# Kernel tuning notes

Hardware: AMD Instinct MI355X
Metric: run time of the kernel (lower is better)

## Reference

```python
import jax, jax.numpy as jnp
import numpy as np

N = 100000   # nodes
E = 3200000  # edges (avg degree 32)
D = 128      # in_dim
RATIO = 0.5
K = int(RATIO * N)  # nodes kept by pooling


def setup_inputs() -> dict:
    key = jax.random.key(0)
    k1, k2, k3 = jax.random.split(key, 3)
    x = jax.random.normal(k1, (N, D), dtype=jnp.float32)
    edge_index = jax.random.randint(k2, (2, E), 0, N, dtype=jnp.int32)
    weight = jax.random.normal(k3, (D, D), dtype=jnp.float32) / np.sqrt(D)
    bias = jnp.zeros((D,), dtype=jnp.float32)
    return {"x": x, "edge_index": edge_index, "weight": weight, "bias": bias}


def gcn_conv(x, edge_index, weight, bias):
    # PyG GCNConv: out = D^{-1/2} (A + I) D^{-1/2} X W + b
    h = x @ weight  # [N, D]
    src, dst = edge_index[0], edge_index[1]
    deg = jax.ops.segment_sum(jnp.ones((E,), h.dtype), dst, num_segments=N) + 1.0  # self-loop
    dinv = jax.lax.rsqrt(deg)  # [N]
    norm = dinv[src] * dinv[dst]  # [E]
    msg = h[src] * norm[:, None]  # gather + scale
    agg = jax.ops.segment_sum(msg, dst, num_segments=N)  # scatter-add
    agg = agg + h * (dinv * dinv)[:, None]  # self-loop contribution
    return agg + bias


def reference(x, edge_index, weight, bias):
    h = gcn_conv(x, edge_index, weight, bias)  # [N, D] node scores/features
    score = jnp.sqrt(jnp.sum(h * h, axis=-1) + 1e-12)  # scalar score per node
    _, perm = jax.lax.top_k(score, K)  # top-k node selection
    x_out = h[perm] * jnp.tanh(score[perm])[:, None]  # gated gather of kept nodes
    # remap / filter edges to the induced subgraph (jit-safe: padded with mask)
    pos = jnp.full((N,), -1, dtype=jnp.int32).at[perm].set(jnp.arange(K, dtype=jnp.int32))
    new_src = pos[edge_index[0]]
    new_dst = pos[edge_index[1]]
    edge_mask = (new_src >= 0) & (new_dst >= 0)
    new_edge_index = jnp.where(edge_mask[None, :], jnp.stack([new_src, new_dst]), -1)
    return x_out, new_edge_index, edge_mask
```

## Files before the change

### kernel.cpp

```cpp
#include <hip/hip_runtime.h>
#include <hip/hip_fp16.h>
#include <stdint.h>

#define NN 100000
#define EE 3200000
#define DD 128
#define KK 50000
#define NB 32768
#define SBLK 128
#define BB 2048
#define NBK 391
#define TILE 8192
#define BMAX 12288
#define NBLK 391

using u16 = unsigned short;
using u32 = unsigned int;
using u64 = unsigned long long;

typedef _Float16 f16x8 __attribute__((ext_vector_type(8)));
typedef float f32x4 __attribute__((ext_vector_type(4)));

__device__ __forceinline__ float bq(float f) {
  u32 b = __float_as_uint(f);
  b += 0x7FFFu + ((b >> 16) & 1u);
  return __uint_as_float(b & 0xFFFF0000u);
}

__device__ __forceinline__ u32 packh2(float a, float b) {
  return (u32)__half_as_ushort(__float2half(a)) |
         ((u32)__half_as_ushort(__float2half(b)) << 16);
}

__global__ void k_init(u32* __restrict__ chist, u32* __restrict__ bcnt,
                       u64* __restrict__ meta, u32* __restrict__ mflag) {
  int i = blockIdx.x * 256 + threadIdx.x;
  for (int j = i; j < NB; j += 256 * 256) bcnt[j] = 0u;
  if (i < NBK) chist[i] = 0u;
  if (i == 0) { meta[0] = ~0ull; meta[1] = 0ull; *mflag = 0u; }
}

__global__ void k_chist(const int* __restrict__ ei, u32* __restrict__ chist) {
  __shared__ u32 cnt[NBK];
  int t = threadIdx.x;
  int e0 = blockIdx.x * TILE;
  int vcnt = EE - e0; if (vcnt > TILE) vcnt = TILE;
  for (int i = t; i < NBK; i += 256) cnt[i] = 0;
  __syncthreads();
  for (int i = t; i < vcnt; i += 256)
    atomicAdd(&cnt[(u32)ei[EE + e0 + i] >> 8], 1u);
  __syncthreads();
  for (int i = t; i < NBK; i += 256)
    if (cnt[i]) atomicAdd(&chist[i], cnt[i]);
}

__global__ void k_cscan(const u32* __restrict__ chist, u32* __restrict__ cbase,
                        u32* __restrict__ pbcur) {
  __shared__ u32 buf[2][512];
  int t = threadIdx.x;
  u32 v = (t < NBK) ? chist[t] : 0u;
  int a = 0; buf[0][t] = v; __syncthreads();
  for (int s = 1; s < 512; s <<= 1) {
    buf[1 - a][t] = buf[a][t] + ((t >= s) ? buf[a][t - s] : 0u);
    a = 1 - a; __syncthreads();
  }
  if (t < NBK) { u32 e = buf[a][t] - v; cbase[t] = e; pbcur[t] = e; }
}

__global__ void k_part1(const int* __restrict__ ei, u32* __restrict__ bcur,
                        u32* __restrict__ ebuf) {
  __shared__ u32 cnt[NBK];
  __shared__ u32 lpos[NBK];
  __shared__ u32 gbase[NBK];
  __shared__ u32 sbuf[TILE];
  __shared__ u16 sbid[TILE];
  int t = threadIdx.x;
  int e0 = blockIdx.x * TILE;
  int vcnt = EE - e0; if (vcnt > TILE) vcnt = TILE;
  for (int i = t; i < NBK; i += 256) cnt[i] = 0;
  __syncthreads();
  for (int i = t; i < vcnt; i += 256) {
    int d = ei[EE + e0 + i];
    atomicAdd(&cnt[d >> 8], 1u);
  }
  __syncthreads();
  if (t < 64) {
    u32 carry = 0;
    for (int c = 0; c < 7; ++c) {
      int idx = c * 64 + t;
      u32 v = (idx < NBK) ? cnt[idx] : 0u;
      u32 x = v;
      #pragma unroll
      for (int s = 1; s < 64; s <<= 1) {
        u32 y = __shfl_up(x, s);
        if (t >= s) x += y;
      }
      if (idx < NBK) lpos[idx] = x - v + carry;
      carry += __shfl(x, 63);
    }
  }
  __syncthreads();
  for (int i = t; i < NBK; i += 256)
    gbase[i] = cnt[i] ? atomicAdd(&bcur[i], cnt[i]) : 0u;
  for (int i = t; i < vcnt; i += 256) {
    int d = ei[EE + e0 + i];
    int s = ei[e0 + i];
    u32 b = (u32)d >> 8;
    u32 p = atomicAdd(&lpos[b], 1u);
    sbuf[p] = ((u32)(d & 255) << 17) | (u32)s;
    sbid[p] = (u16)b;
  }
  __syncthreads();
  for (int i = t; i < vcnt; i += 256) {
    u32 b = sbid[i];
    u32 lstart = lpos[b] - cnt[b];
    ebuf[gbase[b] + ((u32)i - lstart)] = sbuf[i];
  }
}

__global__ void k_part2(const u32* __restrict__ ebuf, const u32* __restrict__ cbase,
                        u32* __restrict__ deg, u32* __restrict__ offs,
                        double* __restrict__ dinv64, float* __restrict__ dinv32,
                        int* __restrict__ csr) {
  __shared__ u32 fcnt[256];
  __shared__ u32 buf[2][256];
  __shared__ u32 ncur[256];
  __shared__ u32 scsr[BMAX];
  int b = blockIdx.x; int t = threadIdx.x;
  int nbase = b * 256;
  u32 gstart = cbase[b];
  u32 gend = (b + 1 < NBK) ? cbase[b + 1] : (u32)EE;
  u32 cnt = gend - gstart;
  fcnt[t] = 0u;
  __syncthreads();
  for (u32 i = t; i < cnt; i += 256)
    atomicAdd(&fcnt[ebuf[gstart + i] >> 17], 1u);
  __syncthreads();
  u32 v = fcnt[t];
  int a = 0; buf[0][t] = v; __syncthreads();
  for (int s = 1; s < 256; s <<= 1) {
    buf[1 - a][t] = buf[a][t] + ((t >= s) ? buf[a][t - s] : 0u);
    a = 1 - a; __syncthreads();
  }
  u32 floc = buf[a][t] - v;
  int node = nbase + t;
  if (node < NN) {
    deg[node] = v;
    offs[node] = gstart + floc;
    double d = 1.0 / sqrt((double)(v + 1u));
    dinv64[node] = d;
    dinv32[node] = (float)d;
  }
  ncur[t] = floc;
  __syncthreads();
  if (cnt <= (u32)BMAX) {
    for (u32 i = t; i < cnt; i += 256) {
      u32 en = ebuf[gstart + i];
      u32 p = atomicAdd(&ncur[en >> 17], 1u);
      scsr[p] = en & 0x1FFFFu;
    }
    __syncthreads();
    for (u32 i = t; i < cnt; i += 256) csr[gstart + i] = (int)scsr[i];
  } else {
    for (u32 i = t; i < cnt; i += 256) {
      u32 en = ebuf[gstart + i];
      u32 p = atomicAdd(&ncur[en >> 17], 1u);
      csr[gstart + p] = (int)(en & 0x1FFFFu);
    }
  }
}

__global__ void k_wfrag(const float* __restrict__ w, f16x8* __restrict__ wfrag) {
  int idx = blockIdx.x * 256 + threadIdx.x;
  int lane = idx & 63;
  int ctt = (idx >> 6) & 7;
  int kstep = idx >> 9;
  int c = ctt * 16 + (lane & 15);
  int kbase = (lane >> 4) * 8 + kstep * 32;
  f16x8 v;
  #pragma unroll
  for (int j = 0; j < 8; ++j) v[j] = (_Float16)w[(kbase + j) * DD + c];
  wfrag[idx] = v;
}

__global__ void __launch_bounds__(256) k_gemm_mfma(const float* __restrict__ x,
                                                   const f16x8* __restrict__ wfrag,
                                                   u16* __restrict__ hW16) {
  int wid = threadIdx.x >> 6, lane = threadIdx.x & 63;
  int rowbase = blockIdx.x * 32 + (wid & 1) * 16;
  int colgrp = wid >> 1;
  int row = rowbase + (lane & 15);
  int klane = (lane >> 4) * 8;

  f32x4 acc[4] = {{0,0,0,0},{0,0,0,0},{0,0,0,0},{0,0,0,0}};
  const float* xr = x + (size_t)row * DD;
  #pragma unroll
  for (int kstep = 0; kstep < 4; ++kstep) {
    const float4* xp = (const float4*)(xr + klane + kstep * 32);
    float4 v0 = xp[0], v1 = xp[1];
    f16x8 a;
    a[0] = (_Float16)v0.x; a[1] = (_Float16)v0.y;
    a[2] = (_Float16)v0.z; a[3] = (_Float16)v0.w;
    a[4] = (_Float16)v1.x; a[5] = (_Float16)v1.y;
    a[6] = (_Float16)v1.z; a[7] = (_Float16)v1.w;
    #pragma unroll
    for (int ct = 0; ct < 4; ++ct) {
      f16x8 b = wfrag[(kstep * 8 + colgrp * 4 + ct) * 64 + lane];
      acc[ct] = __builtin_amdgcn_mfma_f32_16x16x32_f16(a, b, acc[ct], 0, 0, 0);
    }
  }
  #pragma unroll
  for (int ct = 0; ct < 4; ++ct) {
    int col = colgrp * 64 + ct * 16 + (lane & 15);
    #pragma unroll
    for (int reg = 0; reg < 4; ++reg) {
      int r = rowbase + (lane >> 4) * 4 + reg;
      hW16[(size_t)r * DD + col] = __half_as_ushort(__float2half(acc[ct][reg]));
    }
  }
}

__global__ void k_check(const float* __restrict__ x, const float* __restrict__ w,
                        const u16* __restrict__ hW16, u32* __restrict__ flag) {
  int idx = blockIdx.x * 256 + threadIdx.x;
  int r = idx >> 7, c = idx & 127;
  const float4* xr = (const float4*)(x + (size_t)r * DD);
  float acc = 0.0f;
  #pragma unroll 8
  for (int k4 = 0; k4 < 32; ++k4) {
    float4 xv = xr[k4];
    int kb = k4 * 4;
    acc += xv.x * w[kb * DD + c] + xv.y * w[(kb + 1) * DD + c]
         + xv.z * w[(kb + 2) * DD + c] + xv.w * w[(kb + 3) * DD + c];
  }
  float got = __half2float(__ushort_as_half(hW16[r * DD + c]));
  if (fabsf(got - acc) > 0.02f) atomicOr(flag, 1u);
}

__global__ void k_gemm_fb(const float* __restrict__ x, const float* __restrict__ w,
                          u16* __restrict__ hW16, const u32* __restrict__ flag) {
  if (*flag == 0u) return;
  __shared__ float Wl[DD * DD];
  int t = threadIdx.x;
  for (int i = t; i < DD * DD; i += 256) Wl[i] = w[i];
  __syncthreads();
  int c = t & 127, rh = t >> 7;
  for (int it = 0; it < 128; ++it) {
    int r = blockIdx.x * 256 + it * 2 + rh;
    if (r < NN) {
      const float4* xr = (const float4*)(x + (size_t)r * DD);
      float acc = 0.0f;
      #pragma unroll 4
      for (int k4 = 0; k4 < 32; ++k4) {
        float4 xv = xr[k4];
        int kb = k4 * 4;
        acc += xv.x * Wl[kb * DD + c];
        acc += xv.y * Wl[(kb + 1) * DD + c];
        acc += xv.z * Wl[(kb + 2) * DD + c];
        acc += xv.w * Wl[(kb + 3) * DD + c];
      }
      hW16[(size_t)r * DD + c] = __half_as_ushort(__float2half(acc));
    }
  }
}

__global__ void k_agg(const u32* __restrict__ hw, const float* __restrict__ dinv32,
                      const u32* __restrict__ offs, const u32* __restrict__ deg,
                      const int* __restrict__ csr, const float* __restrict__ bias,
                      u32* __restrict__ hc16, u64* __restrict__ key,
                      float* __restrict__ gate) {
  int t = threadIdx.x;
  int l4 = t & 15;
  int node = blockIdx.x * 16 + (t >> 4);
  if (node >= NN) return;
  const uint4* hwp = (const uint4*)hw;
  float di = dinv32[node];
  float a0 = 0.f, a1 = 0.f, a2 = 0.f, a3 = 0.f;
  float a4 = 0.f, a5 = 0.f, a6 = 0.f, a7 = 0.f;
  u32 o = offs[node], cnt = deg[node];
  u32 k = 0;
  for (; k + 2 <= cnt; k += 2) {
    int s0 = csr[o + k], s1 = csr[o + k + 1];
    float n0 = dinv32[s0] * di, n1 = dinv32[s1] * di;
    uint4 w0 = hwp[(size_t)s0 * 16 + l4];
    uint4 w1 = hwp[(size_t)s1 * 16 + l4];
    float2 p00 = __half22float2(*(__half2*)&w0.x), p01 = __half22float2(*(__half2*)&w0.y);
    float2 p02 = __half22float2(*(__half2*)&w0.z), p03 = __half22float2(*(__half2*)&w0.w);
    float2 p10 = __half22float2(*(__half2*)&w1.x), p11 = __half22float2(*(__half2*)&w1.y);
    float2 p12 = __half22float2(*(__half2*)&w1.z), p13 = __half22float2(*(__half2*)&w1.w);
    a0 += p00.x * n0 + p10.x * n1;
    a1 += p00.y * n0 + p10.y * n1;
    a2 += p01.x * n0 + p11.x * n1;
    a3 += p01.y * n0 + p11.y * n1;
    a4 += p02.x * n0 + p12.x * n1;
    a5 += p02.y * n0 + p12.y * n1;
    a6 += p03.x * n0 + p13.x * n1;
    a7 += p03.y * n0 + p13.y * n1;
  }
  for (; k < cnt; ++k) {
    int s = csr[o + k];
    float nrm = dinv32[s] * di;
    uint4 wb = hwp[(size_t)s * 16 + l4];
    float2 p0 = __half22float2(*(__half2*)&wb.x), p1 = __half22float2(*(__half2*)&wb.y);
    float2 p2 = __half22float2(*(__half2*)&wb.z), p3 = __half22float2(*(__half2*)&wb.w);
    a0 += p0.x * nrm; a1 += p0.y * nrm; a2 += p1.x * nrm; a3 += p1.y * nrm;
    a4 += p2.x * nrm; a5 += p2.y * nrm; a6 += p3.x * nrm; a7 += p3.y * nrm;
  }
  float di2 = di * di;
  uint4 wb = hwp[(size_t)node * 16 + l4];
  float2 p0 = __half22float2(*(__half2*)&wb.x), p1 = __half22float2(*(__half2*)&wb.y);
  float2 p2 = __half22float2(*(__half2*)&wb.z), p3 = __half22float2(*(__half2*)&wb.w);
  float4 bv0 = ((const float4*)bias)[2 * l4];
  float4 bv1 = ((const float4*)bias)[2 * l4 + 1];
  a0 += p0.x * di2 + bv0.x;
  a1 += p0.y * di2 + bv0.y;
  a2 += p1.x * di2 + bv0.z;
  a3 += p1.y * di2 + bv0.w;
  a4 += p2.x * di2 + bv1.x;
  a5 += p2.y * di2 + bv1.y;
  a6 += p3.x * di2 + bv1.z;
  a7 += p3.y * di2 + bv1.w;
  uint4 out;
  out.x = packh2(a0, a1); out.y = packh2(a2, a3);
  out.z = packh2(a4, a5); out.w = packh2(a6, a7);
  ((uint4*)hc16)[(size_t)node * 16 + l4] = out;
  float ss = a0 * a0 + a1 * a1 + a2 * a2 + a3 * a3
           + a4 * a4 + a5 * a5 + a6 * a6 + a7 * a7;
  #pragma unroll
  for (int off = 8; off > 0; off >>= 1) ss += __shfl_xor(ss, off);
  if (l4 == 0) {
    u32 sb = __float_as_uint(ss);
    key[node] = ((u64)sb << 17) | (u64)(0x1FFFF - node);
    gate[node] = tanhf(sqrtf(ss + 1e-12f));
  }
}

__global__ void k_minmax(const u64* __restrict__ key, u64* __restrict__ meta) {
  __shared__ u64 smn[256], smx[256];
  int t = threadIdx.x; int i = blockIdx.x * 256 + t;
  u64 v = (i < NN) ? key[i] : key[0];
  smn[t] = v; smx[t] = v; __syncthreads();
  for (int s = 128; s > 0; s >>= 1) {
    if (t < s) {
      if (smn[t + s] < smn[t]) smn[t] = smn[t + s];
      if (smx[t + s] > smx[t]) smx[t] = smx[t + s];
    }
    __syncthreads();
  }
  if (t == 0) { atomicMin(&meta[0], smn[0]); atomicMax(&meta[1], smx[0]); }
}

__device__ __forceinline__ u32 bshift(u64 kmin, u64 kmax) {
  u64 range = kmax - kmin;
  int bits = 64 - __clzll(range | 1ull);
  return (u32)(bits > 15 ? bits - 15 : 0);
}

__global__ void k_hist(const u64* __restrict__ key, const u64* __restrict__ meta,
                       u32* __restrict__ barr, u32* __restrict__ bcnt) {
  int i = blockIdx.x * blockDim.x + threadIdx.x;
  if (i >= NN) return;
  u64 kmin = meta[0];
  u32 sh = bshift(kmin, meta[1]);
  u32 b = (u32)((key[i] - kmin) >> sh);
  barr[i] = b;
  atomicAdd(&bcnt[b], 1u);
}

__global__ void k_scan2(u32* __restrict__ bsum, int nb) {
  __shared__ u32 buf[2][512];
  int t = threadIdx.x;
  u32 v = (t < nb) ? bsum[t] : 0u;
  int a = 0; buf[0][t] = v; __syncthreads();
  for (int s = 1; s < 512; s <<= 1) {
    buf[1 - a][t] = buf[a][t] + ((t >= s) ? buf[a][t - s] : 0u);
    a = 1 - a; __syncthreads();
  }
  if (t < nb) bsum[t] = buf[a][t] - v;
}

__global__ void k_bscan1(const u32* __restrict__ bcnt, u32* __restrict__ bsum2) {
  __shared__ u32 sh[256];
  int t = threadIdx.x; int r = blockIdx.x * 256 + t;
  u32 v = bcnt[NB - 1 - r];
  sh[t] = v; __syncthreads();
  for (int s = 128; s > 0; s >>= 1) { if (t < s) sh[t] += sh[t + s]; __syncthreads(); }
  if (t == 0) bsum2[blockIdx.x] = sh[0];
}

__global__ void k_bscan3(const u32* __restrict__ bcnt, const u32* __restrict__ bsum2,
                         u32* __restrict__ base, u32* __restrict__ bcur) {
  __shared__ u32 buf[2][256];
  int t = threadIdx.x; int r = blockIdx.x * 256 + t;
  int b = NB - 1 - r;
  u32 v = bcnt[b];
  int a = 0; buf[0][t] = v; __syncthreads();
  for (int s = 1; s < 256; s <<= 1) {
    buf[1 - a][t] = buf[a][t] + ((t >= s) ? buf[a][t - s] : 0u);
    a = 1 - a; __syncthreads();
  }
  u32 bs = buf[a][t] - v + bsum2[blockIdx.x];
  base[b] = bs;
  bcur[b] = NN - bs - v;
}

__global__ void k_bscatter(const u32* __restrict__ barr, u32* __restrict__ bcur,
                           u32* __restrict__ blist) {
  int i = blockIdx.x * blockDim.x + threadIdx.x;
  if (i >= NN) return;
  u32 p = atomicAdd(&bcur[barr[i]], 1u);
  blist[p] = (u32)i;
}

__global__ void k_rank2(const u64* __restrict__ key, const u32* __restrict__ barr,
                        const u32* __restrict__ bcnt, const u32* __restrict__ base,
                        const u32* __restrict__ blist, int* __restrict__ arank,
                        u32* __restrict__ bandNode) {
  int i = blockIdx.x * blockDim.x + threadIdx.x;
  if (i >= NN) return;
  u32 b = barr[i];
  u64 ki = key[i];
  u32 bs = base[b], cnt = bcnt[b];
  u32 off = NN - bs - cnt;
  u32 gt = 0;
  for (u32 j = 0; j < cnt; ++j) gt += (key[blist[off + j]] > ki) ? 1u : 0u;
  int r = (int)(bs + gt);
  arank[i] = r;
  int rb = r - (KK - BB);
  if (rb >= 0 && rb < 2 * BB) bandNode[rb] = (u32)i;
}

__global__ void k_bscore(const u32* __restrict__ bandNode,
                         const float* __restrict__ x, const float* __restrict__ w,
                         const double* __restrict__ dinv64,
                         const u32* __restrict__ offs, const u32* __restrict__ deg,
                         const int* __restrict__ csr, const float* __restrict__ bias,
                         u64* __restrict__ ekey) {
  __shared__ double zsh[4][DD];
  int wid = threadIdx.x >> 6;
  int lane = threadIdx.x & 63;
  int slot = blockIdx.x * 4 + wid;
  int node = (int)bandNode[slot];
  double di = dinv64[node];
  double z0 = 0.0, z1 = 0.0;
  u32 o = offs[node], cnt = deg[node];
  for (u32 k = 0; k <= cnt; ++k) {
    int s = (k < cnt) ? csr[o + k] : node;
    double wgt = (k < cnt) ? (dinv64[s] * di) : (di * di);
    float2 xv = ((const float2*)x)[(size_t)s * 64 + lane];
    z0 += (double)xv.x * wgt;
    z1 += (double)xv.y * wgt;
  }
  zsh[wid][2 * lane] = z0;
  zsh[wid][2 * lane + 1] = z1;
  __syncthreads();
  float2 bv = ((const float2*)bias)[lane];
  double a0 = (double)bv.x, a1 = (double)bv.y;
  for (int kk = 0; kk < DD; ++kk) {
    double zk = zsh[wid][kk];
    float2 wv = ((const float2*)w)[kk * 64 + lane];
    a0 += zk * (double)wv.x;
    a1 += zk * (double)wv.y;
  }
  double ss = a0 * a0 + a1 * a1;
  #pragma unroll
  for (int off = 32; off > 0; off >>= 1) ss += __shfl_xor(ss, off);
  if (lane == 0) {
    double sc = sqrt(ss + 1e-12);
    u64 bits = (u64)__double_as_longlong(sc);
    ekey[slot] = (bits & ~0x1FFFFull) | (u64)(0x1FFFF - node);
  }
}

__global__ void k_bandrank(const u64* __restrict__ ekey, u32* __restrict__ brank) {
  __shared__ u64 sk[2 * BB];
  int t = threadIdx.x;
  for (int j = t; j < 2 * BB; j += 256) sk[j] = ekey[j];
  __syncthreads();
  int idx = blockIdx.x * 256 + t;
  u64 kk = sk[idx];
  u32 c = 0;
  for (int j = 0; j < 2 * BB; ++j) c += (sk[j] > kk) ? 1u : 0u;
  brank[idx] = c;
}

__global__ void k_pos2(const int* __restrict__ arank, const u32* __restrict__ brank,
                       int* __restrict__ pos) {
  int i = blockIdx.x * blockDim.x + threadIdx.x;
  if (i >= NN) return;
  int r = arank[i];
  int p;
  if (r < KK - BB) p = r;
  else if (r < KK + BB) {
    u32 br = brank[r - (KK - BB)];
    p = (br < BB) ? (KK - BB + (int)br) : -1;
  } else p = -1;
  pos[i] = p;
}

__global__ void k_xout(const u32* __restrict__ hc16, const float* __restrict__ gate,
                       const int* __restrict__ pos, float* __restrict__ outx) {
  int id = blockIdx.x * blockDim.x + threadIdx.x;
  if (id >= NN * 64) return;
  int i = id >> 6, d2 = id & 63;
  int p = pos[i];
  if (p < 0) return;
  float g = gate[i];
  u32 hv = hc16[(size_t)i * 64 + d2];
  float2 v = __half22float2(*(__half2*)&hv);
  float2 out = make_float2(bq(v.x * g), bq(v.y * g));
  ((float2*)outx)[(size_t)p * 64 + d2] = out;
}

__global__ void k_edges(const int* __restrict__ ei, const int* __restrict__ pos,
                        float* __restrict__ osrc, float* __restrict__ odst,
                        float* __restrict__ omask) {
  int e = blockIdx.x * blockDim.x + threadIdx.x;
  if (e >= EE) return;
  int ns = pos[ei[e]];
  int nd = pos[ei[EE + e]];
  bool m = (ns >= 0) && (nd >= 0);
  osrc[e] = m ? bq((float)ns) : -1.0f;
  odst[e] = m ? bq((float)nd) : -1.0f;
  omask[e] = m ? 1.0f : 0.0f;
}

extern "C" void kernel_launch(void* const* d_in, const int* in_sizes, int n_in,
                              void* d_out, int out_size, void* d_ws, size_t ws_size,
                              hipStream_t stream) {
  const float* x    = (const float*)d_in[0];
  const int*   ei   = (const int*)d_in[1];
  const float* w    = (const float*)d_in[2];
  const float* bias = (const float*)d_in[3];
  float* outx = (float*)d_out;
  char* ws = (char*)d_ws;

  size_t off = 0;
  auto alloc = [&](size_t b) -> void* {
    void* p = ws + off; off += (b + 255) & ~(size_t)255; return p;
  };
  u16*    hW16   = (u16*)alloc((size_t)NN * DD * 2);
  u32*    hc16   = (u32*)alloc((size_t)NN * DD * 2);
  double* dinv64 = (double*)alloc((size_t)NN * 8);
  float*  dinv32 = (float*)alloc((size_t)NN * 4);
  float*  gate   = (float*)alloc((size_t)NN * 4);
  u64*    key    = (u64*)alloc((size_t)NN * 8);
  u32*    deg    = (u32*)alloc((size_t)NN * 4);
  u32*    offs   = (u32*)alloc((size_t)NN * 4);
  int*    csr    = (int*)alloc((size_t)EE * 4);
  u32*    ebuf   = (u32*)alloc((size_t)EE * 4);
  u32*    chist  = (u32*)alloc((size_t)NBK * 4);
  u32*    cbase  = (u32*)alloc((size_t)NBK * 4);
  u32*    pbcur  = (u32*)alloc((size_t)NBK * 4);
  int*    arank  = (int*)alloc((size_t)NN * 4);
  int*    pos    = (int*)alloc((size_t)NN * 4);
  u64*    meta   = (u64*)alloc(4 * 8);
  u32*    bcnt   = (u32*)alloc((size_t)NB * 4);
  u32*    base   = (u32*)alloc((size_t)NB * 4);
  u32*    bcur   = (u32*)alloc((size_t)NB * 4);
  u32*    bsum2  = (u32*)alloc(SBLK * 4);
  u32*    barr   = (u32*)alloc((size_t)NN * 4);
  u32*    blist  = (u32*)alloc((size_t)NN * 4);
  u32*    bandNode = (u32*)alloc((size_t)2 * BB * 4);
  u64*    ekey     = (u64*)alloc((size_t)2 * BB * 8);
  u32*    brank    = (u32*)alloc((size_t)2 * BB * 4);
  f16x8*  wfrag    = (f16x8*)alloc((size_t)2048 * 16);
  u32*    mflag    = (u32*)alloc(256);

  k_init<<<256, 256, 0, stream>>>(chist, bcnt, meta, mflag);
  k_chist<<<(EE + TILE - 1) / TILE, 256, 0, stream>>>(ei, chist);
  k_cscan<<<1, 512, 0, stream>>>(chist, cbase, pbcur);
  k_part1<<<(EE + TILE - 1) / TILE, 256, 0, stream>>>(ei, pbcur, ebuf);
  k_part2<<<NBK, 256, 0, stream>>>(ebuf, cbase, deg, offs, dinv64, dinv32, csr);
  k_wfrag<<<8, 256, 0, stream>>>(w, wfrag);
  k_gemm_mfma<<<NN / 32, 256, 0, stream>>>(x, wfrag, hW16);
  k_check<<<16, 256, 0, stream>>>(x, w, hW16, mflag);
  k_gemm_fb<<<NBLK, 256, 0, stream>>>(x, w, hW16, mflag);
  k_agg<<<(NN + 15) / 16, 256, 0, stream>>>((const u32*)hW16, dinv32, offs, deg, csr,
                                            bias, hc16, key, gate);
  k_minmax<<<NBLK, 256, 0, stream>>>(key, meta);
  k_hist<<<(NN + 255) / 256, 256, 0, stream>>>(key, meta, barr, bcnt);
  k_bscan1<<<SBLK, 256, 0, stream>>>(bcnt, bsum2);
  k_scan2<<<1, 512, 0, stream>>>(bsum2, SBLK);
  k_bscan3<<<SBLK, 256, 0, stream>>>(bcnt, bsum2, base, bcur);
  k_bscatter<<<(NN + 255) / 256, 256, 0, stream>>>(barr, bcur, blist);
  k_rank2<<<(NN + 255) / 256, 256, 0, stream>>>(key, barr, bcnt, base, blist, arank,
                                                bandNode);
  k_bscore<<<(2 * BB) / 4, 256, 0, stream>>>(bandNode, x, w, dinv64, offs, deg, csr,
                                             bias, ekey);
  k_bandrank<<<(2 * BB) / 256, 256, 0, stream>>>(ekey, brank);
  k_pos2<<<(NN + 255) / 256, 256, 0, stream>>>(arank, brank, pos);
  k_xout<<<(NN * 64 + 255) / 256, 256, 0, stream>>>(hc16, gate, pos, outx);
  float* oei = outx + (size_t)KK * DD;
  k_edges<<<(EE + 255) / 256, 256, 0, stream>>>(ei, pos, oei, oei + EE, oei + 2 * (size_t)EE);
}
```

Before: 410.6 us.

## Cut kernel launches by fusing small passes and dropping the GEMM check/fallback

Folds W-fragment packing into the init kernel and the key min/max reduction into the aggregation kernel. Replaces the three-kernel bucket scan with a single 1024-thread scan and computes pos inline in the output and edge kernels instead of materialising it. Removes the fp16 GEMM accuracy check and its fallback kernel. Vectorises the dst histogram loads and edge remapping. Fewer launches and passes over memory, at the cost of losing the precision safety net and running the bucket scan serially in one block.

```diff
diff --git a/kernel.cpp b/kernel.cpp
--- a/kernel.cpp
+++ b/kernel.cpp
@@ -7,12 +7,10 @@
 #define DD 128
 #define KK 50000
 #define NB 32768
-#define SBLK 128
 #define BB 2048
 #define NBK 391
 #define TILE 8192
 #define BMAX 12288
-#define NBLK 391
 
 using u16 = unsigned short;
 using u32 = unsigned int;
@@ -32,12 +30,33 @@
          ((u32)__half_as_ushort(__float2half(b)) << 16);
 }
 
-__global__ void k_init(u32* __restrict__ chist, u32* __restrict__ bcnt,
-                       u64* __restrict__ meta, u32* __restrict__ mflag) {
+__device__ __forceinline__ int posf(int r, const u32* __restrict__ brank) {
+  if (r < KK - BB) return r;
+  if (r < KK + BB) {
+    u32 br = brank[r - (KK - BB)];
+    return (br < BB) ? (KK - BB + (int)br) : -1;
+  }
+  return -1;
+}
+
+__global__ void k_init(const float* __restrict__ w, f16x8* __restrict__ wfrag,
+                       u32* __restrict__ chist, u32* __restrict__ bcnt,
+                       u64* __restrict__ meta) {
   int i = blockIdx.x * 256 + threadIdx.x;
   for (int j = i; j < NB; j += 256 * 256) bcnt[j] = 0u;
   if (i < NBK) chist[i] = 0u;
-  if (i == 0) { meta[0] = ~0ull; meta[1] = 0ull; *mflag = 0u; }
+  if (i == 0) { meta[0] = ~0ull; meta[1] = 0ull; }
+  if (i < 2048) {
+    int lane = i & 63;
+    int ctt = (i >> 6) & 7;
+    int kstep = i >> 9;
+    int c = ctt * 16 + (lane & 15);
+    int kbase = (lane >> 4) * 8 + kstep * 32;
+    f16x8 v;
+    #pragma unroll
+    for (int j = 0; j < 8; ++j) v[j] = (_Float16)w[(kbase + j) * DD + c];
+    wfrag[i] = v;
+  }
 }
 
 __global__ void k_chist(const int* __restrict__ ei, u32* __restrict__ chist) {
@@ -47,8 +66,14 @@
   int vcnt = EE - e0; if (vcnt > TILE) vcnt = TILE;
   for (int i = t; i < NBK; i += 256) cnt[i] = 0;
   __syncthreads();
-  for (int i = t; i < vcnt; i += 256)
-    atomicAdd(&cnt[(u32)ei[EE + e0 + i] >> 8], 1u);
+  const int4* dv = (const int4*)(ei + EE + e0);
+  for (int i = t; i < (vcnt >> 2); i += 256) {
+    int4 d = dv[i];
+    atomicAdd(&cnt[(u32)d.x >> 8], 1u);
+    atomicAdd(&cnt[(u32)d.y >> 8], 1u);
+    atomicAdd(&cnt[(u32)d.z >> 8], 1u);
+    atomicAdd(&cnt[(u32)d.w >> 8], 1u);
+  }
   __syncthreads();
   for (int i = t; i < NBK; i += 256)
     if (cnt[i]) atomicAdd(&chist[i], cnt[i]);
@@ -79,9 +104,13 @@
   int vcnt = EE - e0; if (vcnt > TILE) vcnt = TILE;
   for (int i = t; i < NBK; i += 256) cnt[i] = 0;
   __syncthreads();
-  for (int i = t; i < vcnt; i += 256) {
-    int d = ei[EE + e0 + i];
-    atomicAdd(&cnt[d >> 8], 1u);
+  const int4* dv4 = (const int4*)(ei + EE + e0);
+  for (int i = t; i < (vcnt >> 2); i += 256) {
+    int4 d = dv4[i];
+    atomicAdd(&cnt[(u32)d.x >> 8], 1u);
+    atomicAdd(&cnt[(u32)d.y >> 8], 1u);
+    atomicAdd(&cnt[(u32)d.z >> 8], 1u);
+    atomicAdd(&cnt[(u32)d.w >> 8], 1u);
   }
   __syncthreads();
   if (t < 64) {
@@ -168,19 +197,6 @@
       csr[gstart + p] = (int)(en & 0x1FFFFu);
     }
   }
-}
-
-__global__ void k_wfrag(const float* __restrict__ w, f16x8* __restrict__ wfrag) {
-  int idx = blockIdx.x * 256 + threadIdx.x;
-  int lane = idx & 63;
-  int ctt = (idx >> 6) & 7;
-  int kstep = idx >> 9;
-  int c = ctt * 16 + (lane & 15);
-  int kbase = (lane >> 4) * 8 + kstep * 32;
-  f16x8 v;
-  #pragma unroll
-  for (int j = 0; j < 8; ++j) v[j] = (_Float16)w[(kbase + j) * DD + c];
-  wfrag[idx] = v;
 }
 
 __global__ void __launch_bounds__(256) k_gemm_mfma(const float* __restrict__ x,
@@ -220,59 +236,15 @@
   }
 }
 
-__global__ void k_check(const float* __restrict__ x, const float* __restrict__ w,
-                        const u16* __restrict__ hW16, u32* __restrict__ flag) {
-  int idx = blockIdx.x * 256 + threadIdx.x;
-  int r = idx >> 7, c = idx & 127;
-  const float4* xr = (const float4*)(x + (size_t)r * DD);
-  float acc = 0.0f;
-  #pragma unroll 8
-  for (int k4 = 0; k4 < 32; ++k4) {
-    float4 xv = xr[k4];
-    int kb = k4 * 4;
-    acc += xv.x * w[kb * DD + c] + xv.y * w[(kb + 1) * DD + c]
-         + xv.z * w[(kb + 2) * DD + c] + xv.w * w[(kb + 3) * DD + c];
-  }
-  float got = __half2float(__ushort_as_half(hW16[r * DD + c]));
-  if (fabsf(got - acc) > 0.02f) atomicOr(flag, 1u);
-}
-
-__global__ void k_gemm_fb(const float* __restrict__ x, const float* __restrict__ w,
-                          u16* __restrict__ hW16, const u32* __restrict__ flag) {
-  if (*flag == 0u) return;
-  __shared__ float Wl[DD * DD];
-  int t = threadIdx.x;
-  for (int i = t; i < DD * DD; i += 256) Wl[i] = w[i];
-  __syncthreads();
-  int c = t & 127, rh = t >> 7;
-  for (int it = 0; it < 128; ++it) {
-    int r = blockIdx.x * 256 + it * 2 + rh;
-    if (r < NN) {
-      const float4* xr = (const float4*)(x + (size_t)r * DD);
-      float acc = 0.0f;
-      #pragma unroll 4
-      for (int k4 = 0; k4 < 32; ++k4) {
-        float4 xv = xr[k4];
-        int kb = k4 * 4;
-        acc += xv.x * Wl[kb * DD + c];
-        acc += xv.y * Wl[(kb + 1) * DD + c];
-        acc += xv.z * Wl[(kb + 2) * DD + c];
-        acc += xv.w * Wl[(kb + 3) * DD + c];
-      }
-      hW16[(size_t)r * DD + c] = __half_as_ushort(__float2half(acc));
-    }
-  }
-}
-
 __global__ void k_agg(const u32* __restrict__ hw, const float* __restrict__ dinv32,
                       const u32* __restrict__ offs, const u32* __restrict__ deg,
                       const int* __restrict__ csr, const float* __restrict__ bias,
                       u32* __restrict__ hc16, u64* __restrict__ key,
-                      float* __restrict__ gate) {
+                      float* __restrict__ gate, u64* __restrict__ meta) {
+  __shared__ u64 kmn[16], kmx[16];
   int t = threadIdx.x;
   int l4 = t & 15;
   int node = blockIdx.x * 16 + (t >> 4);
-  if (node >= NN) return;
   const uint4* hwp = (const uint4*)hw;
   float di = dinv32[node];
   float a0 = 0.f, a1 = 0.f, a2 = 0.f, a3 = 0.f;
@@ -330,24 +302,23 @@
   for (int off = 8; off > 0; off >>= 1) ss += __shfl_xor(ss, off);
   if (l4 == 0) {
     u32 sb = __float_as_uint(ss);
-    key[node] = ((u64)sb << 17) | (u64)(0x1FFFF - node);
+    u64 kk = ((u64)sb << 17) | (u64)(0x1FFFF - node);
+    key[node] = kk;
     gate[node] = tanhf(sqrtf(ss + 1e-12f));
-  }
-}
-
-__global__ void k_minmax(const u64* __restrict__ key, u64* __restrict__ meta) {
-  __shared__ u64 smn[256], smx[256];
-  int t = threadIdx.x; int i = blockIdx.x * 256 + t;
-  u64 v = (i < NN) ? key[i] : key[0];
-  smn[t] = v; smx[t] = v; __syncthreads();
-  for (int s = 128; s > 0; s >>= 1) {
-    if (t < s) {
-      if (smn[t + s] < smn[t]) smn[t] = smn[t + s];
-      if (smx[t + s] > smx[t]) smx[t] = smx[t + s];
-    }
-    __syncthreads();
-  }
-  if (t == 0) { atomicMin(&meta[0], smn[0]); atomicMax(&meta[1], smx[0]); }
+    kmn[t >> 4] = kk;
+    kmx[t >> 4] = kk;
+  }
+  __syncthreads();
+  if (t == 0) {
+    u64 mn = ~0ull, mx = 0ull;
+    #pragma unroll
+    for (int g = 0; g < 16; ++g) {
+      if (kmn[g] < mn) mn = kmn[g];
+      if (kmx[g] > mx) mx = kmx[g];
+    }
+    atomicMin(&meta[0], mn);
+    atomicMax(&meta[1], mx);
+  }
 }
 
 __device__ __forceinline__ u32 bshift(u64 kmin, u64 kmax) {
@@ -367,41 +338,28 @@
   atomicAdd(&bcnt[b], 1u);
 }
 
-__global__ void k_scan2(u32* __restrict__ bsum, int nb) {
-  __shared__ u32 buf[2][512];
+__global__ void k_bscan(const u32* __restrict__ bcnt, u32* __restrict__ base,
+                        u32* __restrict__ bcur) {
+  __shared__ u32 buf[2][1024];
   int t = threadIdx.x;
-  u32 v = (t < nb) ? bsum[t] : 0u;
-  int a = 0; buf[0][t] = v; __syncthreads();
-  for (int s = 1; s < 512; s <<= 1) {
-    buf[1 - a][t] = buf[a][t] + ((t >= s) ? buf[a][t - s] : 0u);
-    a = 1 - a; __syncthreads();
-  }
-  if (t < nb) bsum[t] = buf[a][t] - v;
-}
-
-__global__ void k_bscan1(const u32* __restrict__ bcnt, u32* __restrict__ bsum2) {
-  __shared__ u32 sh[256];
-  int t = threadIdx.x; int r = blockIdx.x * 256 + t;
-  u32 v = bcnt[NB - 1 - r];
-  sh[t] = v; __syncthreads();
-  for (int s = 128; s > 0; s >>= 1) { if (t < s) sh[t] += sh[t + s]; __syncthreads(); }
-  if (t == 0) bsum2[blockIdx.x] = sh[0];
-}
-
-__global__ void k_bscan3(const u32* __restrict__ bcnt, const u32* __restrict__ bsum2,
-                         u32* __restrict__ base, u32* __restrict__ bcur) {
-  __shared__ u32 buf[2][256];
-  int t = threadIdx.x; int r = blockIdx.x * 256 + t;
-  int b = NB - 1 - r;
-  u32 v = bcnt[b];
-  int a = 0; buf[0][t] = v; __syncthreads();
-  for (int s = 1; s < 256; s <<= 1) {
-    buf[1 - a][t] = buf[a][t] + ((t >= s) ? buf[a][t - s] : 0u);
-    a = 1 - a; __syncthreads();
-  }
-  u32 bs = buf[a][t] - v + bsum2[blockIdx.x];
-  base[b] = bs;
-  bcur[b] = NN - bs - v;
+  u32 carry = 0;
+  for (int c = 0; c < NB / 1024; ++c) {
+    int r = c * 1024 + t;
+    int b = NB - 1 - r;
+    u32 v = bcnt[b];
+    int a = 0; buf[0][t] = v; __syncthreads();
+    for (int s = 1; s < 1024; s <<= 1) {
+      buf[1 - a][t] = buf[a][t] + ((t >= s) ? buf[a][t - s] : 0u);
+      a = 1 - a; __syncthreads();
+    }
+    u32 inc = buf[a][t];
+    u32 bs = inc - v + carry;
+    base[b] = bs;
+    bcur[b] = NN - bs - v;
+    u32 tot = buf[a][1023];
+    __syncthreads();
+    carry += tot;
+  }
 }
 
 __global__ void k_bscatter(const u32* __restrict__ barr, u32* __restrict__ bcur,
@@ -484,26 +442,13 @@
   brank[idx] = c;
 }
 
-__global__ void k_pos2(const int* __restrict__ arank, const u32* __restrict__ brank,
-                       int* __restrict__ pos) {
-  int i = blockIdx.x * blockDim.x + threadIdx.x;
-  if (i >= NN) return;
-  int r = arank[i];
-  int p;
-  if (r < KK - BB) p = r;
-  else if (r < KK + BB) {
-    u32 br = brank[r - (KK - BB)];
-    p = (br < BB) ? (KK - BB + (int)br) : -1;
-  } else p = -1;
-  pos[i] = p;
-}
-
 __global__ void k_xout(const u32* __restrict__ hc16, const float* __restrict__ gate,
-                       const int* __restrict__ pos, float* __restrict__ outx) {
+                       const int* __restrict__ arank, const u32* __restrict__ brank,
+                       float* __restrict__ outx) {
   int id = blockIdx.x * blockDim.x + threadIdx.x;
   if (id >= NN * 64) return;
   int i = id >> 6, d2 = id & 63;
-  int p = pos[i];
+  int p = posf(arank[i], brank);
   if (p < 0) return;
   float g = gate[i];
   u32 hv = hc16[(size_t)i * 64 + d2];
@@ -512,17 +457,23 @@
   ((float2*)outx)[(size_t)p * 64 + d2] = out;
 }
 
-__global__ void k_edges(const int* __restrict__ ei, const int* __restrict__ pos,
+__global__ void k_edges(const int* __restrict__ ei, const int* __restrict__ arank,
+                        const u32* __restrict__ brank,
                         float* __restrict__ osrc, float* __restrict__ odst,
                         float* __restrict__ omask) {
-  int e = blockIdx.x * blockDim.x + threadIdx.x;
-  if (e >= EE) return;
-  int ns = pos[ei[e]];
-  int nd = pos[ei[EE + e]];
-  bool m = (ns >= 0) && (nd >= 0);
-  osrc[e] = m ? bq((float)ns) : -1.0f;
-  odst[e] = m ? bq((float)nd) : -1.0f;
-  omask[e] = m ? 1.0f : 0.0f;
+  int e2 = blockIdx.x * blockDim.x + threadIdx.x;
+  if (e2 >= EE / 2) return;
+  int2 sv = ((const int2*)ei)[e2];
+  int2 dv = ((const int2*)(ei + EE))[e2];
+  int ps0 = posf(arank[sv.x], brank), pd0 = posf(arank[dv.x], brank);
+  int ps1 = posf(arank[sv.y], brank), pd1 = posf(arank[dv.y], brank);
+  bool m0 = (ps0 >= 0) && (pd0 >= 0);
+  bool m1 = (ps1 >= 0) && (pd1 >= 0);
+  ((float2*)osrc)[e2] = make_float2(m0 ? bq((float)ps0) : -1.0f,
+                                    m1 ? bq((float)ps1) : -1.0f);
+  ((float2*)odst)[e2] = make_float2(m0 ? bq((float)pd0) : -1.0f,
+                                    m1 ? bq((float)pd1) : -1.0f);
+  ((float2*)omask)[e2] = make_float2(m0 ? 1.0f : 0.0f, m1 ? 1.0f : 0.0f);
 }
 
 extern "C" void kernel_launch(void* const* d_in, const int* in_sizes, int n_in,
@@ -553,44 +504,35 @@
   u32*    cbase  = (u32*)alloc((size_t)NBK * 4);
   u32*    pbcur  = (u32*)alloc((size_t)NBK * 4);
   int*    arank  = (int*)alloc((size_t)NN * 4);
-  int*    pos    = (int*)alloc((size_t)NN * 4);
   u64*    meta   = (u64*)alloc(4 * 8);
   u32*    bcnt   = (u32*)alloc((size_t)NB * 4);
   u32*    base   = (u32*)alloc((size_t)NB * 4);
   u32*    bcur   = (u32*)alloc((size_t)NB * 4);
-  u32*    bsum2  = (u32*)alloc(SBLK * 4);
   u32*    barr   = (u32*)alloc((size_t)NN * 4);
   u32*    blist  = (u32*)alloc((size_t)NN * 4);
   u32*    bandNode = (u32*)alloc((size_t)2 * BB * 4);
   u64*    ekey     = (u64*)alloc((size_t)2 * BB * 8);
   u32*    brank    = (u32*)alloc((size_t)2 * BB * 4);
   f16x8*  wfrag    = (f16x8*)alloc((size_t)2048 * 16);
-  u32*    mflag    = (u32*)alloc(256);
-
-  k_init<<<256, 256, 0, stream>>>(chist, bcnt, meta, mflag);
+
+  k_init<<<256, 256, 0, stream>>>(w, wfrag, chist, bcnt, meta);
   k_chist<<<(EE + TILE - 1) / TILE, 256, 0, stream>>>(ei, chist);
   k_cscan<<<1, 512, 0, stream>>>(chist, cbase, pbcur);
   k_part1<<<(EE + TILE - 1) / TILE, 256, 0, stream>>>(ei, pbcur, ebuf);
   k_part2<<<NBK, 256, 0, stream>>>(ebuf, cbase, deg, offs, dinv64, dinv32, csr);
-  k_wfrag<<<8, 256, 0, stream>>>(w, wfrag);
   k_gemm_mfma<<<NN / 32, 256, 0, stream>>>(x, wfrag, hW16);
-  k_check<<<16, 256, 0, stream>>>(x, w, hW16, mflag);
-  k_gemm_fb<<<NBLK, 256, 0, stream>>>(x, w, hW16, mflag);
-  k_agg<<<(NN + 15) / 16, 256, 0, stream>>>((const u32*)hW16, dinv32, offs, deg, csr,
-                                            bias, hc16, key, gate);
-  k_minmax<<<NBLK, 256, 0, stream>>>(key, meta);
+  k_agg<<<NN / 16, 256, 0, stream>>>((const u32*)hW16, dinv32, offs, deg, csr,
+                                     bias, hc16, key, gate, meta);
   k_hist<<<(NN + 255) / 256, 256, 0, stream>>>(key, meta, barr, bcnt);
-  k_bscan1<<<SBLK, 256, 0, stream>>>(bcnt, bsum2);
-  k_scan2<<<1, 512, 0, stream>>>(bsum2, SBLK);
-  k_bscan3<<<SBLK, 256, 0, stream>>>(bcnt, bsum2, base, bcur);
+  k_bscan<<<1, 1024, 0, stream>>>(bcnt, base, bcur);
   k_bscatter<<<(NN + 255) / 256, 256, 0, stream>>>(barr, bcur, blist);
   k_rank2<<<(NN + 255) / 256, 256, 0, stream>>>(key, barr, bcnt, base, blist, arank,
                                                 bandNode);
   k_bscore<<<(2 * BB) / 4, 256, 0, stream>>>(bandNode, x, w, dinv64, offs, deg, csr,
                                              bias, ekey);
   k_bandrank<<<(2 * BB) / 256, 256, 0, stream>>>(ekey, brank);
-  k_pos2<<<(NN + 255) / 256, 256, 0, stream>>>(arank, brank, pos);
-  k_xout<<<(NN * 64 + 255) / 256, 256, 0, stream>>>(hc16, gate, pos, outx);
+  k_xout<<<(NN * 64 + 255) / 256, 256, 0, stream>>>(hc16, gate, arank, brank, outx);
   float* oei = outx + (size_t)KK * DD;
-  k_edges<<<(EE + 255) / 256, 256, 0, stream>>>(ei, pos, oei, oei + EE, oei + 2 * (size_t)EE);
-}
+  k_edges<<<(EE / 2 + 255) / 256, 256, 0, stream>>>(ei, arank, brank, oei, oei + EE,
+                                                    oei + 2 * (size_t)EE);
+}
```

After: 509.7 us. 24.1% more time.
